# Performance work log

Hardware: AMD Instinct MI355X
Metric: run time of the kernel (lower is better)

## Reference

```python
import jax, jax.numpy as jnp
import numpy as np

RF = 3          # receptive_field_size (cubic)
STRIDE = 1
TEMP = 1.0      # softmax temperature ('soft' sampling, eval mode: no Gumbel noise)
TREE_DEPTH = 4

# Truth table of all 16 binary gates: GATES[g, t] = value of gate g on input
# pattern t = 2*a + b (a = first child, b = second child), t in {0,1,2,3}.
GATES = np.array([[(g >> t) & 1 for t in range(4)] for g in range(16)],
                 dtype=np.float32)  # (16, 4)


def _lut_eval(a, b, w):
    """Differentiable 2-input LUT. a, b: (B,K,P,nodes); w: (nodes,K,16)."""
    probs = jax.nn.softmax(w / TEMP, axis=-1)          # (nodes,K,16)
    lut = probs @ jnp.asarray(GATES)                   # (nodes,K,4) relaxed truth table
    lut = jnp.moveaxis(lut, 0, 1)[:, None]             # (K,1,nodes,4) -> bcast over B,P
    l0, l1, l2, l3 = lut[..., 0], lut[..., 1], lut[..., 2], lut[..., 3]
    na, nb = 1.0 - a, 1.0 - b
    # E[lut(a,b)] under independent Bernoulli inputs
    return l0 * na * nb + l1 * na * b + l2 * a * nb + l3 * a * b


def setup_inputs() -> dict:
    key = jax.random.key(0)
    ks = jax.random.split(key, 8)
    B, C, H, W, D = 4, 3, 32, 32, 32
    K, S = 32, 16  # num_kernels, lut_rank**tree_depth leaves
    x = jax.random.uniform(ks[0], (B, C, H, W, D), dtype=jnp.float32)
    # (lut_rank=2, K, S, 4) coords (h, w, d, c); rf=3 and channels=3 so all in [0,3)
    kernel_coords = jax.random.randint(ks[1], (2, K, S, 4), 0, 3, dtype=jnp.int32)
    w0 = jax.random.normal(ks[2], (16, K, 16), dtype=jnp.float32)
    w1 = jax.random.normal(ks[3], (8, K, 16), dtype=jnp.float32)
    w2 = jax.random.normal(ks[4], (4, K, 16), dtype=jnp.float32)
    w3 = jax.random.normal(ks[5], (2, K, 16), dtype=jnp.float32)
    w4 = jax.random.normal(ks[6], (1, K, 16), dtype=jnp.float32)
    return {"x": x, "kernel_coords": kernel_coords,
            "w0": w0, "w1": w1, "w2": w2, "w3": w3, "w4": w4}


def reference(x, kernel_coords, w0, w1, w2, w3, w4):
    B, C, H, W, D = x.shape
    OH, OW, OD = (H - RF) // STRIDE + 1, (W - RF) // STRIDE + 1, (D - RF) // STRIDE + 1
    kc = kernel_coords
    # linear offset of each leaf coord inside flattened (C,H,W,D) volume
    base = ((kc[..., 3] * H + kc[..., 0]) * W + kc[..., 1]) * D + kc[..., 2]  # (2,K,S)
    oh = jnp.arange(OH) * STRIDE
    ow = jnp.arange(OW) * STRIDE
    od = jnp.arange(OD) * STRIDE
    patch = ((oh[:, None, None] * W + ow[None, :, None]) * D
             + od[None, None, :]).reshape(-1)                                  # (P,)
    lin = base[:, :, None, :] + patch[None, None, :, None]                     # (2,K,P,S)
    g = x.reshape(B, -1)[:, lin]                                               # (B,2,K,P,S)
    out = _lut_eval(g[:, 0], g[:, 1], w0)                                      # (B,K,P,S)
    for w in (w1, w2, w3, w4):  # binary tree reduction over TREE_DEPTH levels
        out = _lut_eval(out[..., 0::2], out[..., 1::2], w)
    return out.reshape(B, out.shape[1], OH, OW, OD)
```

## Files before the change

### kernel.cpp

```cpp
#include <hip/hip_runtime.h>


#define B_  4
#define C_  3
#define H_  32
#define W_  32
#define D_  32
#define K_  32
#define S_  16
#define TPB 256

typedef float v4f __attribute__((ext_vector_type(4), aligned(4)));

__device__ __forceinline__ v4f lut4(v4f a, v4f b, float l0, float d1, float d2, float d3) {
    v4f t = a * d2 + l0;
    t = b * d1 + t;
    t = (a * b) * d3 + t;
    return t;
}

__global__ __launch_bounds__(TPB, 4) void logic_conv3d(
    const float* __restrict__ x,
    const int*   __restrict__ kc,
    const float* __restrict__ w0,
    const float* __restrict__ w1,
    const float* __restrict__ w2,
    const float* __restrict__ w3,
    const float* __restrict__ w4,
    float*       __restrict__ out)
{
    __shared__ float4 s_lut[31];
    __shared__ int    s_lb[32];

    const int bk  = blockIdx.x;
    const int oh  = blockIdx.y;
    const int b   = bk >> 5;
    const int k   = bk & 31;
    const int tid = threadIdx.x;

    if (tid < 31) {
        const float* wp; int ln;
        if      (tid < 16) { wp = w0; ln = tid;      }
        else if (tid < 24) { wp = w1; ln = tid - 16; }
        else if (tid < 28) { wp = w2; ln = tid - 24; }
        else if (tid < 30) { wp = w3; ln = tid - 28; }
        else               { wp = w4; ln = 0;        }
        const float* wrow = wp + (ln * K_ + k) * 16;
        float lg[16];
        float m = -1e30f;
        #pragma unroll
        for (int g = 0; g < 16; ++g) { lg[g] = wrow[g]; m = fmaxf(m, lg[g]); }
        float z = 0.f;
        #pragma unroll
        for (int g = 0; g < 16; ++g) { lg[g] = __expf(lg[g] - m); z += lg[g]; }
        const float inv = 1.0f / z;
        float l0 = 0.f, l1 = 0.f, l2 = 0.f, l3 = 0.f;
        #pragma unroll
        for (int g = 0; g < 16; ++g) {
            float p = lg[g] * inv;
            if (g & 1) l0 += p;
            if (g & 2) l1 += p;
            if (g & 4) l2 += p;
            if (g & 8) l3 += p;
        }
        s_lut[tid] = make_float4(l0, l1 - l0, l2 - l0, (l3 - l2) - (l1 - l0));
    } else if (tid >= 32 && tid < 64) {
        const int idx  = tid - 32;
        const int tree = idx >> 4;
        const int s    = idx & 15;
        const int off  = ((tree * K_ + k) * S_ + s) * 4;
        const int h = kc[off + 0], w = kc[off + 1], d = kc[off + 2], c = kc[off + 3];
        s_lb[idx] = ((c * H_ + h) * W_ + w) * D_ + d;
    }
    __syncthreads();

    int sA[16], sB[16];
    #pragma unroll
    for (int s = 0; s < 16; ++s) {
        sA[s] = __builtin_amdgcn_readfirstlane(s_lb[s]);
        sB[s] = __builtin_amdgcn_readfirstlane(s_lb[16 + s]);
    }

    const float* xb2 = x + (size_t)b * (C_ * H_ * W_ * D_) + oh * (W_ * D_);

    const int g   = tid & 7;
    int ow        = tid >> 3;
    if (ow > 29) ow = 29;
    const int od0 = (g < 7) ? (g << 2) : 26;
    const int vo  = ow * D_ + od0;

    v4f v[16];
    #pragma unroll
    for (int s = 0; s < 16; ++s) {
        const v4f A = *(const v4f*)(xb2 + sA[s] + vo);
        const v4f Bv = *(const v4f*)(xb2 + sB[s] + vo);
        const float4 L = s_lut[s];
        v[s] = lut4(A, Bv, L.x, L.y, L.z, L.w);
    }

    #pragma unroll
    for (int lvl = 0; lvl < 4; ++lvl) {
        const int width = 8 >> lvl;
        const int nbase = (lvl == 0) ? 16 : (lvl == 1) ? 24 : (lvl == 2) ? 28 : 30;
        #pragma unroll
        for (int j = 0; j < width; ++j) {
            const float4 L = s_lut[nbase + j];
            v[j] = lut4(v[2 * j], v[2 * j + 1], L.x, L.y, L.z, L.w);
        }
    }

    float* outp = out + (size_t)bk * 27000 + oh * 900 + ow * 30 + od0;
    *(v4f*)outp = v[0];
}

extern "C" void kernel_launch(void* const* d_in, const int* in_sizes, int n_in,
                              void* d_out, int out_size, void* d_ws, size_t ws_size,
                              hipStream_t stream) {
    const float* x  = (const float*)d_in[0];
    const int*   kc = (const int*)d_in[1];
    const float* w0 = (const float*)d_in[2];
    const float* w1 = (const float*)d_in[3];
    const float* w2 = (const float*)d_in[4];
    const float* w3 = (const float*)d_in[5];
    const float* w4 = (const float*)d_in[6];
    float* out = (float*)d_out;

    dim3 grid(B_ * K_, 30);
    logic_conv3d<<<grid, TPB, 0, stream>>>(x, kc, w0, w1, w2, w3, w4, out);
}
```

Before: 87.53 us.

## Process 8 outputs per thread and two output rows per block

Each thread now computes eight consecutive depth outputs with 8-wide vectors instead of four, and each block covers two output rows, which halves the grid. The first tree level is fused into the leaf loop so only 8 intermediate vectors stay live instead of 16. This amortises the per-block softmax/LUT setup and index reads over twice the work and raises per-thread work, at the cost of fewer blocks, more overlapping (redundant) edge lanes, and possible register pressure (launch bound relaxed to 3 blocks per SM).

```diff
diff --git a/kernel.cpp b/kernel.cpp
--- a/kernel.cpp
+++ b/kernel.cpp
@@ -10,16 +10,16 @@
 #define S_  16
 #define TPB 256
 
-typedef float v4f __attribute__((ext_vector_type(4), aligned(4)));
+typedef float v8f __attribute__((ext_vector_type(8), aligned(4)));
 
-__device__ __forceinline__ v4f lut4(v4f a, v4f b, float l0, float d1, float d2, float d3) {
-    v4f t = a * d2 + l0;
+__device__ __forceinline__ v8f lut8(v8f a, v8f b, float l0, float d1, float d2, float d3) {
+    v8f t = a * d2 + l0;
     t = b * d1 + t;
     t = (a * b) * d3 + t;
     return t;
 }
 
-__global__ __launch_bounds__(TPB, 4) void logic_conv3d(
+__global__ __launch_bounds__(TPB, 3) void logic_conv3d(
     const float* __restrict__ x,
     const int*   __restrict__ kc,
     const float* __restrict__ w0,
@@ -33,7 +33,6 @@
     __shared__ int    s_lb[32];
 
     const int bk  = blockIdx.x;
-    const int oh  = blockIdx.y;
     const int b   = bk >> 5;
     const int k   = bk & 31;
     const int tid = threadIdx.x;
@@ -81,36 +80,50 @@
         sB[s] = __builtin_amdgcn_readfirstlane(s_lb[16 + s]);
     }
 
-    const float* xb2 = x + (size_t)b * (C_ * H_ * W_ * D_) + oh * (W_ * D_);
+    const int g   = tid & 3;
+    const int woi = tid >> 2;
+    const int ohl = woi >> 5;
+    int ow        = woi & 31;
+    if (ow > 29) ow = 29;
+    const int od0 = (g < 3) ? (g << 3) : 22;
+    const int oh  = blockIdx.y * 2 + ohl;
+    const int vo  = ohl * (W_ * D_) + ow * D_ + od0;
 
-    const int g   = tid & 7;
-    int ow        = tid >> 3;
-    if (ow > 29) ow = 29;
-    const int od0 = (g < 7) ? (g << 2) : 26;
-    const int vo  = ow * D_ + od0;
+    const float* xb2 = x + (size_t)b * (C_ * H_ * W_ * D_) + (blockIdx.y * 2) * (W_ * D_);
 
-    v4f v[16];
+    v8f v1[8];
     #pragma unroll
-    for (int s = 0; s < 16; ++s) {
-        const v4f A = *(const v4f*)(xb2 + sA[s] + vo);
-        const v4f Bv = *(const v4f*)(xb2 + sB[s] + vo);
-        const float4 L = s_lut[s];
-        v[s] = lut4(A, Bv, L.x, L.y, L.z, L.w);
+    for (int j = 0; j < 8; ++j) {
+        const int s0 = 2 * j, s1 = 2 * j + 1;
+        const v8f A0 = *(const v8f*)(xb2 + sA[s0] + vo);
+        const v8f B0 = *(const v8f*)(xb2 + sB[s0] + vo);
+        const float4 L0 = s_lut[s0];
+        const v8f t0 = lut8(A0, B0, L0.x, L0.y, L0.z, L0.w);
+        const v8f A1 = *(const v8f*)(xb2 + sA[s1] + vo);
+        const v8f B1 = *(const v8f*)(xb2 + sB[s1] + vo);
+        const float4 L1 = s_lut[s1];
+        const v8f t1 = lut8(A1, B1, L1.x, L1.y, L1.z, L1.w);
+        const float4 LN = s_lut[16 + j];
+        v1[j] = lut8(t0, t1, LN.x, LN.y, LN.z, LN.w);
     }
 
     #pragma unroll
-    for (int lvl = 0; lvl < 4; ++lvl) {
-        const int width = 8 >> lvl;
-        const int nbase = (lvl == 0) ? 16 : (lvl == 1) ? 24 : (lvl == 2) ? 28 : 30;
-        #pragma unroll
-        for (int j = 0; j < width; ++j) {
-            const float4 L = s_lut[nbase + j];
-            v[j] = lut4(v[2 * j], v[2 * j + 1], L.x, L.y, L.z, L.w);
-        }
+    for (int j = 0; j < 4; ++j) {
+        const float4 L = s_lut[24 + j];
+        v1[j] = lut8(v1[2 * j], v1[2 * j + 1], L.x, L.y, L.z, L.w);
+    }
+    #pragma unroll
+    for (int j = 0; j < 2; ++j) {
+        const float4 L = s_lut[28 + j];
+        v1[j] = lut8(v1[2 * j], v1[2 * j + 1], L.x, L.y, L.z, L.w);
+    }
+    {
+        const float4 L = s_lut[30];
+        v1[0] = lut8(v1[0], v1[1], L.x, L.y, L.z, L.w);
     }
 
     float* outp = out + (size_t)bk * 27000 + oh * 900 + ow * 30 + od0;
-    *(v4f*)outp = v[0];
+    *(v8f*)outp = v1[0];
 }
 
 extern "C" void kernel_launch(void* const* d_in, const int* in_sizes, int n_in,
@@ -125,6 +138,6 @@
     const float* w4 = (const float*)d_in[6];
     float* out = (float*)d_out;
 
-    dim3 grid(B_ * K_, 30);
+    dim3 grid(B_ * K_, 15);
     logic_conv3d<<<grid, TPB, 0, stream>>>(x, kc, w0, w1, w2, w3, w4, out);
 }
```

Result: slower. 89.81 us (+2.6%).
